# Kernel tuning notes

Hardware: AMD Instinct MI355X
Metric: run time of the kernel (lower is better)

The kernel has to match this reference:

```python
import jax, jax.numpy as jnp
import numpy as np
import math

B, T_IN, T_COND, D, H, W = 2, 2048, 1024, 1024, 16, 512
HD = D // H
NEG = -1e9


def setup_inputs() -> dict:
    key = jax.random.key(0)
    ks = jax.random.split(key, 6)
    scale = 0.02
    x = jax.random.normal(ks[0], (B, T_IN, D), dtype=jnp.float32)
    condition = jax.random.normal(ks[1], (B, T_COND, D), dtype=jnp.float32)
    end_inds = jax.random.randint(ks[2], (B,), W, min(T_IN, T_COND), dtype=jnp.int32)
    in_proj_w = jax.random.normal(ks[3], (3 * D, D), dtype=jnp.float32) * scale
    in_proj_b = jnp.zeros((3 * D,), dtype=jnp.float32)
    out_w = jax.random.normal(ks[4], (D, D), dtype=jnp.float32) * scale
    out_b = jnp.zeros((D,), dtype=jnp.float32)
    return {"x": x, "condition": condition, "end_inds": end_inds,
            "in_proj_w": in_proj_w, "in_proj_b": in_proj_b,
            "out_w": out_w, "out_b": out_b}


def _window_mask(end_inds, t_in, t_cond):
    # allowed keys: index in [end - W, end) within each of the two segments
    e = end_inds[:, None].astype(jnp.int32)
    idx_in = jnp.arange(t_in, dtype=jnp.int32)[None, :]
    idx_c = jnp.arange(t_cond, dtype=jnp.int32)[None, :]
    m_in = (idx_in >= e - W) & (idx_in < e)
    m_c = (idx_c >= e - W) & (idx_c < e)
    return jnp.concatenate([m_in, m_c], axis=1)  # (B, S)


def reference(x, condition, end_inds, in_proj_w, in_proj_b, out_w, out_b):
    inp = jnp.concatenate([x, condition], axis=1)          # (B, S, D)
    S = inp.shape[1]
    qkv = inp @ in_proj_w.T + in_proj_b                     # (B, S, 3D)
    q, k, v = jnp.split(qkv, 3, axis=-1)
    # (B, H, S, HD)
    q = q.reshape(B, S, H, HD).transpose(0, 2, 1, 3)
    k = k.reshape(B, S, H, HD).transpose(0, 2, 1, 3)
    v = v.reshape(B, S, H, HD).transpose(0, 2, 1, 3)
    scores = jnp.einsum('bhqd,bhkd->bhqk', q, k) / math.sqrt(HD)
    mask = _window_mask(end_inds, x.shape[1], condition.shape[1])  # (B, S)
    scores = jnp.where(mask[:, None, None, :], scores, NEG)
    attn = jax.nn.softmax(scores, axis=-1)
    out = jnp.einsum('bhqk,bhkd->bhqd', attn, v)            # (B, H, S, HD)
    out = out.transpose(0, 2, 1, 3).reshape(B, S, D)
    return out @ out_w.T + out_b
```

## Files before the change

kernel.cpp:

```cpp
#include <hip/hip_runtime.h>
#include <stdint.h>

#define TIN   2048
#define TCOND 1024
#define SEQ   3072
#define NB    2
#define NH    16
#define DM    1024
#define HDIM  64
#define WIN   512
#define MROWS (NB*SEQ)
#define NQKV  (3*DM)

typedef float  floatx4 __attribute__((ext_vector_type(4)));
typedef short  bf16x8  __attribute__((ext_vector_type(8)));

__device__ __forceinline__ unsigned short f2bf(float f) {
    unsigned int u = __float_as_uint(f);
    u += 0x7fffu + ((u >> 16) & 1u);
    return (unsigned short)(u >> 16);
}

__device__ __forceinline__ unsigned int pack2bf(float a, float b) {
    return (unsigned int)f2bf(a) | ((unsigned int)f2bf(b) << 16);
}

__device__ __forceinline__ void gl2lds16(const void* g, void* l) {
    __builtin_amdgcn_global_load_lds(
        (const __attribute__((address_space(1))) unsigned int*)g,
        (__attribute__((address_space(3))) unsigned int*)l, 16, 0, 0);
}

__global__ __launch_bounds__(256) void prep(const float* __restrict__ x,
                                            const float* __restrict__ cond,
                                            const float* __restrict__ w_in,
                                            const float* __restrict__ w_out,
                                            unsigned short* __restrict__ inp,
                                            unsigned short* __restrict__ wi_bf,
                                            unsigned short* __restrict__ wo_bf) {
    if (blockIdx.x < 6144) {
        int v = blockIdx.x * 256 + threadIdx.x;
        int m  = v >> 8;
        int d4 = v & 255;
        int bb = (m >= SEQ) ? 1 : 0;
        int s  = m - bb * SEQ;
        const float* src = (s < TIN)
            ? x    + ((size_t)(bb * TIN   + s)        ) * DM + d4 * 4
            : cond + ((size_t)(bb * TCOND + (s - TIN))) * DM + d4 * 4;
        float4 f = *(const float4*)src;
        ushort4 u;
        u.x = f2bf(f.x); u.y = f2bf(f.y); u.z = f2bf(f.z); u.w = f2bf(f.w);
        *(ushort4*)(inp + (size_t)v * 4) = u;
    } else {
        int v = (blockIdx.x - 6144) * 256 + threadIdx.x;
        const float* src; unsigned short* dst; int idx;
        if (v < 786432) { src = w_in;  dst = wi_bf; idx = v; }
        else            { src = w_out; dst = wo_bf; idx = v - 786432; }
        float4 f = *(const float4*)(src + (size_t)idx * 4);
        ushort4 u;
        u.x = f2bf(f.x); u.y = f2bf(f.y); u.z = f2bf(f.z); u.w = f2bf(f.w);
        *(ushort4*)(dst + (size_t)idx * 4) = u;
    }
}

__global__ __launch_bounds__(256, 4) void gemm_qkv(
        const unsigned short* __restrict__ A, const unsigned short* __restrict__ Bt,
        const float* __restrict__ bias,
        unsigned short* __restrict__ q_ws, unsigned short* __restrict__ k_ws,
        unsigned short* __restrict__ vt_ws) {
    __shared__ unsigned short smem[2 * 8192];
    const int K = 1024;
    const int tid  = threadIdx.x;
    const int wave = tid >> 6, lane = tid & 63;
    const int quad = lane >> 4, c16 = lane & 15;
    const int wr = wave >> 1, wc = wave & 1;
    const int m0 = blockIdx.y * 128, n0 = blockIdx.x * 128;

    const unsigned short* gA[2];
    const unsigned short* gB[2];
    int ldst[2];
#pragma unroll
    for (int i = 0; i < 2; i++) {
        int flat = i * 256 + tid;
        int pr = flat >> 2, cp = flat & 3;
        int gc = cp ^ ((pr >> 1) & 3);
        gA[i] = A  + (size_t)(m0 + pr) * K + (gc << 3);
        gB[i] = Bt + (size_t)(n0 + pr) * K + (gc << 3);
        ldst[i] = (i * 256 + wave * 64) * 8;
    }

    floatx4 acc[4][4];
#pragma unroll
    for (int i = 0; i < 4; i++)
#pragma unroll
        for (int j = 0; j < 4; j++) acc[i][j] = (floatx4){0.f, 0.f, 0.f, 0.f};

#pragma unroll
    for (int i = 0; i < 2; i++) {
        gl2lds16(gA[i], &smem[ldst[i]]);
        gl2lds16(gB[i], &smem[4096 + ldst[i]]);
    }

#pragma unroll 2
    for (int it = 0; it < 32; ++it) {
        __syncthreads();
        if (it + 1 < 32) {
            int bo = ((it + 1) & 1) * 8192;
            int k0 = (it + 1) << 5;
#pragma unroll
            for (int i = 0; i < 2; i++) {
                gl2lds16(gA[i] + k0, &smem[bo + ldst[i]]);
                gl2lds16(gB[i] + k0, &smem[bo + 4096 + ldst[i]]);
            }
        }
        const unsigned short* As = &smem[(it & 1) * 8192];
        const unsigned short* Bs = As + 4096;
        bf16x8 af[4], bfr[4];
#pragma unroll
        for (int t = 0; t < 4; t++) {
            int ra = wr * 64 + t * 16 + c16;
            int rb = wc * 64 + t * 16 + c16;
            af[t]  = *(const bf16x8*)&As[ra * 32 + ((quad ^ ((ra >> 1) & 3)) << 3)];
            bfr[t] = *(const bf16x8*)&Bs[rb * 32 + ((quad ^ ((rb >> 1) & 3)) << 3)];
        }
#pragma unroll
        for (int mt = 0; mt < 4; mt++)
#pragma unroll
            for (int nt = 0; nt < 4; nt++)
                acc[mt][nt] = __builtin_amdgcn_mfma_f32_16x16x32_bf16(
                    af[mt], bfr[nt], acc[mt][nt], 0, 0, 0);
    }

    const int which = n0 >> 10;
    const int h0 = (n0 >> 6) & 15;
    if (which == 2) {
#pragma unroll
        for (int mt = 0; mt < 4; mt++) {
            int m = m0 + wr * 64 + mt * 16 + quad * 4;
            int bb = (m >= SEQ) ? 1 : 0;
            int s = m - bb * SEQ;
#pragma unroll
            for (int nt = 0; nt < 4; nt++) {
                int gn = n0 + wc * 64 + nt * 16 + c16;
                float bi = bias[gn];
                int h = (gn >> 6) & 15, hd = gn & 63;
                uint2 w;
                w.x = pack2bf(acc[mt][nt][0] + bi, acc[mt][nt][1] + bi);
                w.y = pack2bf(acc[mt][nt][2] + bi, acc[mt][nt][3] + bi);
                *(uint2*)&vt_ws[((size_t)(bb * NH + h) * HDIM + hd) * SEQ + s] = w;
            }
        }
    } else {
        unsigned short* dstb = (which == 0) ? q_ws : k_ws;
        const float qs = (which == 0) ? 0.125f : 1.0f;
#pragma unroll
        for (int mt = 0; mt < 4; mt++) {
            __syncthreads();
#pragma unroll
            for (int nt = 0; nt < 4; nt++) {
                int col = wc * 64 + nt * 16 + c16;
                float bi = bias[n0 + col];
#pragma unroll
                for (int r = 0; r < 4; r++)
                    smem[(wr * 16 + quad * 4 + r) * 136 + col] =
                        f2bf((acc[mt][nt][r] + bi) * qs);
            }
            __syncthreads();
#pragma unroll
            for (int p = 0; p < 2; p++) {
                int flat = p * 256 + tid;
                int row = flat >> 4, seg = flat & 15;
                bf16x8 v = *(const bf16x8*)&smem[row * 136 + seg * 8];
                int m = m0 + (row >> 4) * 64 + mt * 16 + (row & 15);
                int bb = (m >= SEQ) ? 1 : 0;
                int s = m - bb * SEQ;
                int h = h0 + (seg >> 3);
                *(bf16x8*)&dstb[((size_t)(bb * NH + h) * SEQ + s) * HDIM + (seg & 7) * 8] = v;
            }
        }
    }
}

__global__ __launch_bounds__(256, 4) void gemm_out(
        const unsigned short* __restrict__ A, const unsigned short* __restrict__ Bt,
        const float* __restrict__ bias, float* __restrict__ outp) {
    __shared__ unsigned short smem[2 * 6144];
    const int K = 1024;
    const int tid  = threadIdx.x;
    const int wave = tid >> 6, lane = tid & 63;
    const int quad = lane >> 4, c16 = lane & 15;
    const int wr = wave >> 1, wc = wave & 1;
    const int m0 = blockIdx.y * 64, n0 = blockIdx.x * 128;

    const unsigned short* gA;
    int ldstA;
    {
        int pr = tid >> 2, cp = tid & 3;
        int gc = cp ^ ((pr >> 1) & 3);
        gA = A + (size_t)(m0 + pr) * K + (gc << 3);
        ldstA = wave * 64 * 8;
    }
    const unsigned short* gB[2];
    int ldstB[2];
#pragma unroll
    for (int i = 0; i < 2; i++) {
        int flat = i * 256 + tid;
        int pr = flat >> 2, cp = flat & 3;
        int gc = cp ^ ((pr >> 1) & 3);
        gB[i] = Bt + (size_t)(n0 + pr) * K + (gc << 3);
        ldstB[i] = 2048 + (i * 256 + wave * 64) * 8;
    }

    floatx4 acc[2][4];
#pragma unroll
    for (int i = 0; i < 2; i++)
#pragma unroll
        for (int j = 0; j < 4; j++) acc[i][j] = (floatx4){0.f, 0.f, 0.f, 0.f};

    gl2lds16(gA, &smem[ldstA]);
    gl2lds16(gB[0], &smem[ldstB[0]]);
    gl2lds16(gB[1], &smem[ldstB[1]]);

#pragma unroll 2
    for (int it = 0; it < 32; ++it) {
        __syncthreads();
        if (it + 1 < 32) {
            int bo = ((it + 1) & 1) * 6144;
            int k0 = (it + 1) << 5;
            gl2lds16(gA + k0, &smem[bo + ldstA]);
            gl2lds16(gB[0] + k0, &smem[bo + ldstB[0]]);
            gl2lds16(gB[1] + k0, &smem[bo + ldstB[1]]);
        }
        const unsigned short* As = &smem[(it & 1) * 6144];
        const unsigned short* Bs = As + 2048;
        bf16x8 af[2], bfr[4];
#pragma unroll
        for (int t = 0; t < 2; t++) {
            int ra = wr * 32 + t * 16 + c16;
            af[t] = *(const bf16x8*)&As[ra * 32 + ((quad ^ ((ra >> 1) & 3)) << 3)];
        }
#pragma unroll
        for (int t = 0; t < 4; t++) {
            int rb = wc * 64 + t * 16 + c16;
            bfr[t] = *(const bf16x8*)&Bs[rb * 32 + ((quad ^ ((rb >> 1) & 3)) << 3)];
        }
#pragma unroll
        for (int mt = 0; mt < 2; mt++)
#pragma unroll
            for (int nt = 0; nt < 4; nt++)
                acc[mt][nt] = __builtin_amdgcn_mfma_f32_16x16x32_bf16(
                    af[mt], bfr[nt], acc[mt][nt], 0, 0, 0);
    }

    float* smf = (float*)smem;
#pragma unroll
    for (int mt = 0; mt < 2; mt++) {
        __syncthreads();
#pragma unroll
        for (int nt = 0; nt < 4; nt++) {
            int col = wc * 64 + nt * 16 + c16;
            float bi = bias[n0 + col];
#pragma unroll
            for (int r = 0; r < 4; r++)
                smf[(wr * 16 + quad * 4 + r) * 132 + col] = acc[mt][nt][r] + bi;
        }
        __syncthreads();
#pragma unroll
        for (int p = 0; p < 4; p++) {
            int flat = p * 256 + tid;
            int row = flat >> 5, seg = flat & 31;
            float4 v = *(const float4*)&smf[row * 132 + seg * 4];
            int m = m0 + (row >> 4) * 32 + mt * 16 + (row & 15);
            *(float4*)&outp[(size_t)m * DM + n0 + seg * 4] = v;
        }
    }
}

__global__ __launch_bounds__(256, 4) void attn_kernel(
        const unsigned short* __restrict__ Q, const unsigned short* __restrict__ K,
        const unsigned short* __restrict__ Vt, const int* __restrict__ end_inds,
        unsigned short* __restrict__ O) {
    __shared__ unsigned short smem[2 * 8192];

    const int tid  = threadIdx.x;
    const int wave = tid >> 6, lane = tid & 63;
    const int quad = lane >> 4, c16 = lane & 15;
    const int qt = blockIdx.x, h = blockIdx.y, b = blockIdx.z;
    const int bh = b * NH + h;
    const int e  = end_inds[b];
    const int qbase = qt * 128 + wave * 32;

    const unsigned short* Qp = Q + ((size_t)bh * SEQ + qbase) * HDIM;
    bf16x8 bq[2][2];
#pragma unroll
    for (int qi = 0; qi < 2; qi++)
#pragma unroll
        for (int kk = 0; kk < 2; kk++)
            bq[qi][kk] = *(const bf16x8*)&Qp[(qi * 16 + c16) * HDIM + kk * 32 + quad * 8];

    float l_run[2] = {0.f, 0.f};
    floatx4 accO[2][4];
#pragma unroll
    for (int qi = 0; qi < 2; qi++)
#pragma unroll
        for (int t = 0; t < 4; t++) accO[qi][t] = (floatx4){0.f, 0.f, 0.f, 0.f};

    int k_src[2], v_src[2], dst_off[2];
#pragma unroll
    for (int i = 0; i < 2; i++) {
        int flat = i * 256 + tid;
        int pr = flat >> 3, cp = flat & 7;
        int m5 = pr & 31;
        int kl = (pr & ~31) + (((m5 & 15) >> 2) << 3) + (m5 & 3) + ((m5 >> 4) << 2);
        k_src[i] = kl * HDIM + ((cp ^ (pr & 7)) << 3);
        v_src[i] = pr * SEQ + ((cp ^ (pr & 7)) << 3);
        dst_off[i] = (i * 256 + wave * 64) * 8;
    }

    const unsigned short* Kbase = K  + (size_t)bh * SEQ * HDIM;
    const unsigned short* Vbase = Vt + (size_t)bh * HDIM * SEQ;

    {
        int s0 = e - WIN;
#pragma unroll
        for (int i = 0; i < 2; i++) {
            gl2lds16(Kbase + (size_t)s0 * HDIM + k_src[i], &smem[dst_off[i]]);
            gl2lds16(Vbase + s0 + v_src[i], &smem[4096 + dst_off[i]]);
        }
    }

    for (int ch = 0; ch < 16; ch++) {
        __syncthreads();
        if (ch + 1 < 16) {
            int bo = ((ch + 1) & 1) * 8192;
            int cn = ch + 1;
            int s0 = (cn < 8) ? (e - WIN + cn * 64) : (TIN + e - WIN + (cn - 8) * 64);
#pragma unroll
            for (int i = 0; i < 2; i++) {
                gl2lds16(Kbase + (size_t)s0 * HDIM + k_src[i], &smem[bo + dst_off[i]]);
                gl2lds16(Vbase + s0 + v_src[i], &smem[bo + 4096 + dst_off[i]]);
            }
        }
        const unsigned short* Ks = &smem[(ch & 1) * 8192];
        const unsigned short* Vs = Ks + 4096;

#pragma unroll
        for (int u = 0; u < 2; u++) {
            unsigned int pb[2][4];
#pragma unroll
            for (int sub = 0; sub < 2; sub++) {
                int prow = u * 32 + sub * 16 + c16;
                int sw = c16 & 7;
                bf16x8 ka0 = *(const bf16x8*)&Ks[prow * 64 + (( quad      ^ sw) << 3)];
                bf16x8 ka1 = *(const bf16x8*)&Ks[prow * 64 + (((quad + 4) ^ sw) << 3)];
#pragma unroll
                for (int qi = 0; qi < 2; qi++) {
                    floatx4 z = (floatx4){0.f, 0.f, 0.f, 0.f};
                    z = __builtin_amdgcn_mfma_f32_16x16x32_bf16(ka0, bq[qi][0], z, 0, 0, 0);
                    z = __builtin_amdgcn_mfma_f32_16x16x32_bf16(ka1, bq[qi][1], z, 0, 0, 0);
                    float p0 = __expf(z[0]), p1 = __expf(z[1]);
                    float p2 = __expf(z[2]), p3 = __expf(z[3]);
                    l_run[qi] += (p0 + p1) + (p2 + p3);
                    pb[qi][sub * 2 + 0] = pack2bf(p0, p1);
                    pb[qi][sub * 2 + 1] = pack2bf(p2, p3);
                }
            }
#pragma unroll
            for (int t = 0; t < 4; t++) {
                int vrow = t * 16 + c16;
                bf16x8 va = *(const bf16x8*)&Vs[vrow * 64 +
                                                (((u * 4 + quad) ^ (vrow & 7)) << 3)];
#pragma unroll
                for (int qi = 0; qi < 2; qi++)
                    accO[qi][t] = __builtin_amdgcn_mfma_f32_16x16x32_bf16(
                        va, *(const bf16x8*)&pb[qi][0], accO[qi][t], 0, 0, 0);
            }
        }
    }

    float inv[2];
#pragma unroll
    for (int qi = 0; qi < 2; qi++) {
        float l = l_run[qi];
        l += __shfl_xor(l, 16, 64);
        l += __shfl_xor(l, 32, 64);
        inv[qi] = 1.f / l;
    }

    __syncthreads();
    unsigned short* Os = smem + wave * (32 * 72);
#pragma unroll
    for (int qi = 0; qi < 2; qi++)
#pragma unroll
        for (int t = 0; t < 4; t++) {
            uint2 w;
            w.x = pack2bf(accO[qi][t][0] * inv[qi], accO[qi][t][1] * inv[qi]);
            w.y = pack2bf(accO[qi][t][2] * inv[qi], accO[qi][t][3] * inv[qi]);
            *(uint2*)&Os[(qi * 16 + c16) * 72 + t * 16 + quad * 4] = w;
        }
    __syncthreads();
#pragma unroll
    for (int pass = 0; pass < 4; pass++) {
        int rq = pass * 8 + (lane >> 3);
        int part = lane & 7;
        bf16x8 v = *(const bf16x8*)&Os[rq * 72 + part * 8];
        int s = qbase + rq;
        *(bf16x8*)&O[((size_t)b * SEQ + s) * DM + h * HDIM + part * 8] = v;
    }
}

extern "C" void kernel_launch(void* const* d_in, const int* in_sizes, int n_in,
                              void* d_out, int out_size, void* d_ws, size_t ws_size,
                              hipStream_t stream) {
    const float* x      = (const float*)d_in[0];
    const float* cond   = (const float*)d_in[1];
    const int*   e_inds = (const int*)d_in[2];
    const float* w_in   = (const float*)d_in[3];
    const float* b_in   = (const float*)d_in[4];
    const float* w_out  = (const float*)d_in[5];
    const float* b_out  = (const float*)d_in[6];
    float* out = (float*)d_out;

    char* ws = (char*)d_ws;
    unsigned short* inp_bf = (unsigned short*)(ws);
    unsigned short* wi_bf  = (unsigned short*)(ws + 12582912);
    unsigned short* wo_bf  = (unsigned short*)(ws + 18874368);
    unsigned short* q_ws   = (unsigned short*)(ws + 20971520);
    unsigned short* k_ws   = (unsigned short*)(ws + 33554432);
    unsigned short* vt_ws  = (unsigned short*)(ws + 46137344);
    unsigned short* o_bf   = inp_bf;

    prep<<<10240, 256, 0, stream>>>(x, cond, w_in, w_out, inp_bf, wi_bf, wo_bf);
    gemm_qkv<<<dim3(NQKV / 128, MROWS / 128), 256, 0, stream>>>(
        inp_bf, wi_bf, b_in, q_ws, k_ws, vt_ws);
    attn_kernel<<<dim3(SEQ / 128, NH, NB), 256, 0, stream>>>(
        q_ws, k_ws, vt_ws, e_inds, o_bf);
    gemm_out<<<dim3(DM / 128, MROWS / 64), 256, 0, stream>>>(
        o_bf, wo_bf, b_out, out);
}
```

Measured before the change: 211.5 us.

## Compute K and V projections only for rows inside the attention window

The QKV GEMM grid is rebuilt so that Q is still projected for every row, while K and V are projected only for the 1024 windowed key rows per batch (512 from each segment). These rows are written into compact per-head buffers. The attention kernel then reads contiguous K/V chunks and no longer needs end_inds. This removes about two thirds of the K and V projection FLOPs plus their writes, at the cost of per-block index logic that depends on end_inds.

```diff
diff --git a/kernel.cpp b/kernel.cpp
--- a/kernel.cpp
+++ b/kernel.cpp
@@ -9,8 +9,8 @@
 #define DM    1024
 #define HDIM  64
 #define WIN   512
+#define KW    1024
 #define MROWS (NB*SEQ)
-#define NQKV  (3*DM)
 
 typedef float  floatx4 __attribute__((ext_vector_type(4)));
 typedef short  bf16x8  __attribute__((ext_vector_type(8)));
@@ -65,7 +65,7 @@
 
 __global__ __launch_bounds__(256, 4) void gemm_qkv(
         const unsigned short* __restrict__ A, const unsigned short* __restrict__ Bt,
-        const float* __restrict__ bias,
+        const float* __restrict__ bias, const int* __restrict__ end_inds,
         unsigned short* __restrict__ q_ws, unsigned short* __restrict__ k_ws,
         unsigned short* __restrict__ vt_ws) {
     __shared__ unsigned short smem[2 * 8192];
@@ -74,7 +74,21 @@
     const int wave = tid >> 6, lane = tid & 63;
     const int quad = lane >> 4, c16 = lane & 15;
     const int wr = wave >> 1, wc = wave & 1;
-    const int m0 = blockIdx.y * 128, n0 = blockIdx.x * 128;
+    const int yb = blockIdx.y;
+    const int which = (yb < 48) ? 0 : ((yb < 64) ? 1 : 2);
+    const int n0c = blockIdx.x * 128;
+
+    int m0, batch = 0, jj = 0;
+    if (which == 0) {
+        m0 = yb * 128;
+    } else {
+        int j = yb - (which == 1 ? 48 : 64);
+        batch = j >> 3; jj = j & 7;
+        int e = end_inds[batch];
+        int seg = (jj < 4) ? 0 : 1;
+        int off = (jj & 3) * 128;
+        m0 = batch * SEQ + seg * TIN + (e - WIN) + off;
+    }
 
     const unsigned short* gA[2];
     const unsigned short* gB[2];
@@ -85,7 +99,7 @@
         int pr = flat >> 2, cp = flat & 3;
         int gc = cp ^ ((pr >> 1) & 3);
         gA[i] = A  + (size_t)(m0 + pr) * K + (gc << 3);
-        gB[i] = Bt + (size_t)(n0 + pr) * K + (gc << 3);
+        gB[i] = Bt + (size_t)(which * DM + n0c + pr) * K + (gc << 3);
         ldst[i] = (i * 256 + wave * 64) * 8;
     }
 
@@ -131,35 +145,33 @@
                     af[mt], bfr[nt], acc[mt][nt], 0, 0, 0);
     }
 
-    const int which = n0 >> 10;
-    const int h0 = (n0 >> 6) & 15;
+    const int h0 = n0c >> 6;
     if (which == 2) {
 #pragma unroll
         for (int mt = 0; mt < 4; mt++) {
-            int m = m0 + wr * 64 + mt * 16 + quad * 4;
-            int bb = (m >= SEQ) ? 1 : 0;
-            int s = m - bb * SEQ;
+            int kw = jj * 128 + wr * 64 + mt * 16 + quad * 4;
 #pragma unroll
             for (int nt = 0; nt < 4; nt++) {
-                int gn = n0 + wc * 64 + nt * 16 + c16;
-                float bi = bias[gn];
-                int h = (gn >> 6) & 15, hd = gn & 63;
+                int gn = n0c + wc * 64 + nt * 16 + c16;
+                float bi = bias[2 * DM + gn];
+                int h = gn >> 6, hd = gn & 63;
                 uint2 w;
                 w.x = pack2bf(acc[mt][nt][0] + bi, acc[mt][nt][1] + bi);
                 w.y = pack2bf(acc[mt][nt][2] + bi, acc[mt][nt][3] + bi);
-                *(uint2*)&vt_ws[((size_t)(bb * NH + h) * HDIM + hd) * SEQ + s] = w;
+                *(uint2*)&vt_ws[((size_t)(batch * NH + h) * HDIM + hd) * KW + kw] = w;
             }
         }
     } else {
         unsigned short* dstb = (which == 0) ? q_ws : k_ws;
         const float qs = (which == 0) ? 0.125f : 1.0f;
+        const int bofs = which * DM;
 #pragma unroll
         for (int mt = 0; mt < 4; mt++) {
             __syncthreads();
 #pragma unroll
             for (int nt = 0; nt < 4; nt++) {
                 int col = wc * 64 + nt * 16 + c16;
-                float bi = bias[n0 + col];
+                float bi = bias[bofs + n0c + col];
 #pragma unroll
                 for (int r = 0; r < 4; r++)
                     smem[(wr * 16 + quad * 4 + r) * 136 + col] =
@@ -171,11 +183,18 @@
                 int flat = p * 256 + tid;
                 int row = flat >> 4, seg = flat & 15;
                 bf16x8 v = *(const bf16x8*)&smem[row * 136 + seg * 8];
-                int m = m0 + (row >> 4) * 64 + mt * 16 + (row & 15);
-                int bb = (m >= SEQ) ? 1 : 0;
-                int s = m - bb * SEQ;
+                int ml = (row >> 4) * 64 + mt * 16 + (row & 15);
                 int h = h0 + (seg >> 3);
-                *(bf16x8*)&dstb[((size_t)(bb * NH + h) * SEQ + s) * HDIM + (seg & 7) * 8] = v;
+                size_t ridx;
+                if (which == 0) {
+                    int m = m0 + ml;
+                    int bb = (m >= SEQ) ? 1 : 0;
+                    int s = m - bb * SEQ;
+                    ridx = (size_t)(bb * NH + h) * SEQ + s;
+                } else {
+                    ridx = (size_t)(batch * NH + h) * KW + (jj * 128 + ml);
+                }
+                *(bf16x8*)&dstb[ridx * HDIM + (seg & 7) * 8] = v;
             }
         }
     }
@@ -277,8 +296,8 @@
 }
 
 __global__ __launch_bounds__(256, 4) void attn_kernel(
-        const unsigned short* __restrict__ Q, const unsigned short* __restrict__ K,
-        const unsigned short* __restrict__ Vt, const int* __restrict__ end_inds,
+        const unsigned short* __restrict__ Q, const unsigned short* __restrict__ Kc,
+        const unsigned short* __restrict__ Vtc,
         unsigned short* __restrict__ O) {
     __shared__ unsigned short smem[2 * 8192];
 
@@ -287,7 +306,6 @@
     const int quad = lane >> 4, c16 = lane & 15;
     const int qt = blockIdx.x, h = blockIdx.y, b = blockIdx.z;
     const int bh = b * NH + h;
-    const int e  = end_inds[b];
     const int qbase = qt * 128 + wave * 32;
 
     const unsigned short* Qp = Q + ((size_t)bh * SEQ + qbase) * HDIM;
@@ -313,28 +331,24 @@
         int m5 = pr & 31;
         int kl = (pr & ~31) + (((m5 & 15) >> 2) << 3) + (m5 & 3) + ((m5 >> 4) << 2);
         k_src[i] = kl * HDIM + ((cp ^ (pr & 7)) << 3);
-        v_src[i] = pr * SEQ + ((cp ^ (pr & 7)) << 3);
+        v_src[i] = pr * KW + ((cp ^ (pr & 7)) << 3);
         dst_off[i] = (i * 256 + wave * 64) * 8;
     }
 
-    const unsigned short* Kbase = K  + (size_t)bh * SEQ * HDIM;
-    const unsigned short* Vbase = Vt + (size_t)bh * HDIM * SEQ;
-
-    {
-        int s0 = e - WIN;
-#pragma unroll
-        for (int i = 0; i < 2; i++) {
-            gl2lds16(Kbase + (size_t)s0 * HDIM + k_src[i], &smem[dst_off[i]]);
-            gl2lds16(Vbase + s0 + v_src[i], &smem[4096 + dst_off[i]]);
-        }
+    const unsigned short* Kbase = Kc  + (size_t)bh * KW * HDIM;
+    const unsigned short* Vbase = Vtc + (size_t)bh * HDIM * KW;
+
+#pragma unroll
+    for (int i = 0; i < 2; i++) {
+        gl2lds16(Kbase + k_src[i], &smem[dst_off[i]]);
+        gl2lds16(Vbase + v_src[i], &smem[4096 + dst_off[i]]);
     }
 
     for (int ch = 0; ch < 16; ch++) {
         __syncthreads();
         if (ch + 1 < 16) {
             int bo = ((ch + 1) & 1) * 8192;
-            int cn = ch + 1;
-            int s0 = (cn < 8) ? (e - WIN + cn * 64) : (TIN + e - WIN + (cn - 8) * 64);
+            int s0 = (ch + 1) * 64;
 #pragma unroll
             for (int i = 0; i < 2; i++) {
                 gl2lds16(Kbase + (size_t)s0 * HDIM + k_src[i], &smem[bo + dst_off[i]]);
@@ -427,14 +441,14 @@
     unsigned short* wo_bf  = (unsigned short*)(ws + 18874368);
     unsigned short* q_ws   = (unsigned short*)(ws + 20971520);
     unsigned short* k_ws   = (unsigned short*)(ws + 33554432);
-    unsigned short* vt_ws  = (unsigned short*)(ws + 46137344);
+    unsigned short* vt_ws  = (unsigned short*)(ws + 37748736);
     unsigned short* o_bf   = inp_bf;
 
     prep<<<10240, 256, 0, stream>>>(x, cond, w_in, w_out, inp_bf, wi_bf, wo_bf);
-    gemm_qkv<<<dim3(NQKV / 128, MROWS / 128), 256, 0, stream>>>(
-        inp_bf, wi_bf, b_in, q_ws, k_ws, vt_ws);
+    gemm_qkv<<<dim3(8, 80), 256, 0, stream>>>(
+        inp_bf, wi_bf, b_in, e_inds, q_ws, k_ws, vt_ws);
     attn_kernel<<<dim3(SEQ / 128, NH, NB), 256, 0, stream>>>(
-        q_ws, k_ws, vt_ws, e_inds, o_bf);
+        q_ws, k_ws, vt_ws, o_bf);
     gemm_out<<<dim3(DM / 128, MROWS / 64), 256, 0, stream>>>(
         o_bf, wo_bf, b_out, out);
 }
```

Result: faster. 189.2 us (-10.5%).
